# Kernel tuning notes

Hardware: AMD Instinct MI355X
Metric: run time of the kernel (lower is better)

## Reference

```python
import jax, jax.numpy as jnp
import numpy as np

E = 1024
H = 16
N, S, T = 4, 2048, 2048


def setup_inputs() -> dict:
    key = jax.random.key(0)
    ks = jax.random.split(key, 11)
    scale = 1.0 / np.sqrt(E)
    inp = {
        "query": jax.random.normal(ks[0], (N, S, E), jnp.float32),
        "key": jax.random.normal(ks[1], (N, T, E), jnp.float32),
        "value": jax.random.normal(ks[2], (N, T, E), jnp.float32),
        "Wq": jax.random.normal(ks[3], (E, E), jnp.float32) * scale,
        "bq": jax.random.normal(ks[4], (E,), jnp.float32) * 0.01,
        "Wk": jax.random.normal(ks[5], (E, E), jnp.float32) * scale,
        "bk": jax.random.normal(ks[6], (E,), jnp.float32) * 0.01,
        "Wv": jax.random.normal(ks[7], (E, E), jnp.float32) * scale,
        "bv": jax.random.normal(ks[8], (E,), jnp.float32) * 0.01,
        "Wp": jax.random.normal(ks[9], (E, E), jnp.float32) * scale,
        "bp": jax.random.normal(ks[10], (E,), jnp.float32) * 0.01,
    }
    return inp


def reference(query, key, value, Wq, bq, Wk, bk, Wv, bv, Wp, bp):
    n, s, e = query.shape
    t = value.shape[1]
    hd = e // H
    # Linear projections (torch Linear: x @ W^T + b), split into heads -> [N,H,S,hd]
    Q = (query @ Wq.T + bq).reshape(n, s, H, hd).transpose(0, 2, 1, 3)
    K = (key @ Wk.T + bk).reshape(n, t, H, hd).transpose(0, 2, 1, 3)
    V = (value @ Wv.T + bv).reshape(n, t, H, hd).transpose(0, 2, 1, 3)
    scale = 1.0 / jnp.sqrt(jnp.asarray(hd, Q.dtype))
    attn = jnp.einsum("nhsd,nhtd->nhst", Q, K) * scale  # [N,H,S,T]
    A = jax.nn.softmax(attn, axis=-1)
    Y = jnp.einsum("nhst,nhtd->nhsd", A, V)  # [N,H,S,hd]
    Y = Y.transpose(0, 2, 1, 3).reshape(n, s, e)
    return Y @ Wp.T + bp
```

## Files before the change

kernel.cpp:

```cpp
#include <hip/hip_runtime.h>
#include <hip/hip_bf16.h>
#include <stdint.h>


#define E_DIM 1024
#define H_NUM 16
#define HD 64
#define NB 4
#define SEQ 2048
#define NTOK (NB * SEQ)

typedef __bf16 bf16x8 __attribute__((ext_vector_type(8)));
typedef float f32x4 __attribute__((ext_vector_type(4)));
typedef float f32x16 __attribute__((ext_vector_type(16)));
typedef unsigned short u16;

#define MFMA16(a, b, c) __builtin_amdgcn_mfma_f32_16x16x32_bf16(a, b, c, 0, 0, 0)
#define MFMA32(a, b, c) __builtin_amdgcn_mfma_f32_32x32x16_bf16(a, b, c, 0, 0, 0)

#define VMCNT(n) asm volatile("s_waitcnt vmcnt(" #n ")" ::: "memory")
#define BAR() __builtin_amdgcn_s_barrier()
#define PRIO1() __builtin_amdgcn_s_setprio(1)
#define PRIO0() __builtin_amdgcn_s_setprio(0)

__device__ __forceinline__ u16 f2bf(float f) {
  unsigned int u = __builtin_bit_cast(unsigned int, f);
  unsigned int r = (u + 0x7FFFu + ((u >> 16) & 1u)) >> 16;
  return (u16)r;
}

__device__ __forceinline__ float fexp2(float x) {
  return __builtin_amdgcn_exp2f(x);
}

__device__ __forceinline__ void gload_lds16(const void* g, void* l) {
  __builtin_amdgcn_global_load_lds((const __attribute__((address_space(1))) void*)g,
                                   (__attribute__((address_space(3))) void*)l,
                                   16, 0, 0);
}

__device__ __forceinline__ unsigned cvtpk(float lo, float hi2) {
  unsigned w;
  asm("v_cvt_pk_bf16_f32 %0, %1, %2" : "=v"(w) : "v"(lo), "v"(hi2));
  return w;
}
__device__ __forceinline__ void plswap(unsigned& a, unsigned& b) {
  asm("v_permlane32_swap_b32 %0, %1" : "+v"(a), "+v"(b));
}

template <int B0>
__device__ __forceinline__ bf16x8 packpa(const f32x16& pe) {
  unsigned wa = cvtpk(pe[B0 + 0], pe[B0 + 1]);
  unsigned wb = cvtpk(pe[B0 + 4], pe[B0 + 5]);
  unsigned wc2 = cvtpk(pe[B0 + 2], pe[B0 + 3]);
  unsigned wd = cvtpk(pe[B0 + 6], pe[B0 + 7]);
  plswap(wa, wb);
  plswap(wc2, wd);
  union { unsigned u[4]; bf16x8 v; } pa;
  pa.u[0] = wa; pa.u[1] = wc2; pa.u[2] = wb; pa.u[3] = wd;
  return pa.v;
}

__global__ __launch_bounds__(256) void cvt7(const float* __restrict__ s0,
                                            const float* __restrict__ s1,
                                            const float* __restrict__ s2,
                                            const float* __restrict__ s3,
                                            const float* __restrict__ s4,
                                            const float* __restrict__ s5,
                                            const float* __restrict__ s6,
                                            u16* d0, u16* d1, u16* d2, u16* d3,
                                            u16* d4, u16* d5, u16* d6,
                                            int nbig, int nsmall) {
  const int t = blockIdx.y;
  const float* in;
  u16* out;
  int n4;
  switch (t) {
    case 0: in = s0; out = d0; n4 = nbig; break;
    case 1: in = s1; out = d1; n4 = nbig; break;
    case 2: in = s2; out = d2; n4 = nbig; break;
    case 3: in = s3; out = d3; n4 = nsmall; break;
    case 4: in = s4; out = d4; n4 = nsmall; break;
    case 5: in = s5; out = d5; n4 = nsmall; break;
    default: in = s6; out = d6; n4 = nsmall; break;
  }
  int idx = blockIdx.x * 256 + threadIdx.x;
  int stride = gridDim.x * 256;
  for (int i = idx; i < n4; i += stride) {
    float4 v = ((const float4*)in)[i];
    ushort4 o;
    o.x = f2bf(v.x); o.y = f2bf(v.y); o.z = f2bf(v.z); o.w = f2bf(v.w);
    ((ushort4*)out)[i] = o;
  }
}

__device__ __forceinline__ void rdA(bf16x8 (&af)[4][2], const char* pA, int off,
                                    int cs0, int cs1) {
#pragma unroll
  for (int mi = 0; mi < 4; mi++) {
    af[mi][0] = *(const bf16x8*)(pA + off + mi * 2048 + cs0);
    af[mi][1] = *(const bf16x8*)(pA + off + mi * 2048 + cs1);
  }
}
__device__ __forceinline__ void rdB(bf16x8 (&bfr)[2][2], const char* pB, int off,
                                    int cs0, int cs1) {
#pragma unroll
  for (int nj = 0; nj < 2; nj++) {
    bfr[nj][0] = *(const bf16x8*)(pB + off + nj * 2048 + cs0);
    bfr[nj][1] = *(const bf16x8*)(pB + off + nj * 2048 + cs1);
  }
}
template <int MI0, int NJ0>
__device__ __forceinline__ void mm16(f32x4 (&acc)[8][4], bf16x8 (&af)[4][2],
                                     bf16x8 (&bfr)[2][2]) {
#pragma unroll
  for (int kk = 0; kk < 2; kk++)
#pragma unroll
    for (int mi = 0; mi < 4; mi++)
#pragma unroll
      for (int nj = 0; nj < 2; nj++)
        acc[MI0 + mi][NJ0 + nj] = MFMA16(af[mi][kk], bfr[nj][kk], acc[MI0 + mi][NJ0 + nj]);
}

#define G8_SETUP(Amat, Wmat)                                                          \
  extern __shared__ char LDS[];                                                       \
  const int tid = threadIdx.x;                                                        \
  const int w = tid >> 6, l = tid & 63;                                               \
  const int lr = l & 15, lg = l >> 4;                                                 \
  const int wr = w >> 2, wc2 = w & 3;                                                 \
  const int m0 = blockIdx.x * 256;                                                    \
  const int n0g = blockIdx.y * 256;                                                   \
  const int swz = (lr & 7) << 4;                                                      \
  const int cs0 = (lg << 4) ^ swz;                                                    \
  const int cs1 = ((lg << 4) + 64) ^ swz;                                             \
  const char* pA = LDS + (wr * 16384 + lr * 128);                                     \
  const char* pB = LDS + (65536 + (wc2 >> 1) * 16384 + ((wc2 & 1) * 64 + lr) * 128);  \
  const int sr0 = tid >> 3;                                                           \
  const int sc = (((tid & 7) * 16) ^ ((sr0 & 7) << 4)) >> 1;                          \
  const u16* aS[2];                                                                   \
  const u16* bS[2];                                                                   \
  _Pragma("unroll") for (int ld = 0; ld < 2; ld++) {                                  \
    aS[ld] = (Amat) + (size_t)(m0 + ld * 64 + sr0) * E_DIM + sc;                      \
    bS[ld] = (Wmat) + (size_t)(n0g + ld * 64 + sr0) * E_DIM + sc;                     \
  }                                                                                   \
  f32x4 acc[8][4] = {};                                                               \
  bf16x8 af[4][2], bfr[2][2];

#define STG_A(h, kt)                                                                   \
  do {                                                                                 \
    const int _b = (kt) & 1;                                                           \
    gload_lds16(aS[0] + (h) * 131072 + (size_t)(kt) * 64,                              \
                LDS + _b * 32768 + (h) * 16384 + w * 1024);                            \
    gload_lds16(aS[1] + (h) * 131072 + (size_t)(kt) * 64,                              \
                LDS + _b * 32768 + (h) * 16384 + w * 1024 + 8192);                     \
  } while (0)
#define STG_B(h, kt)                                                                   \
  do {                                                                                 \
    const int _b = (kt) & 1;                                                           \
    gload_lds16(bS[0] + (h) * 131072 + (size_t)(kt) * 64,                              \
                LDS + 65536 + _b * 32768 + (h) * 16384 + w * 1024);                    \
    gload_lds16(bS[1] + (h) * 131072 + (size_t)(kt) * 64,                              \
                LDS + 65536 + _b * 32768 + (h) * 16384 + w * 1024 + 8192);             \
  } while (0)

#define FRAME(T, LAST)                                                                 \
  do {                                                                                 \
    rdA(af, pA, 0, cs0, cs1); rdB(bfr, pB, 0, cs0, cs1);                               \
    STG_B(0, (T) + 1);                                                                 \
    BAR(); PRIO1(); mm16<0, 0>(acc, af, bfr); PRIO0(); BAR();                          \
    rdB(bfr, pB, 4096, cs0, cs1);                                                      \
    STG_B(1, (T) + 1);                                                                 \
    BAR(); PRIO1(); mm16<0, 2>(acc, af, bfr); PRIO0(); BAR();                          \
    rdA(af, pA, 8192, cs0, cs1);                                                       \
    STG_A(1, (T) + 1);                                                                 \
    BAR(); PRIO1(); mm16<4, 2>(acc, af, bfr); PRIO0(); BAR();                          \
    rdB(bfr, pB, 0, cs0, cs1);                                                         \
    if (!(LAST)) { STG_A(0, (T) + 2); VMCNT(2); } else { VMCNT(0); }                   \
    BAR(); PRIO1(); mm16<4, 0>(acc, af, bfr); PRIO0(); BAR();                          \
    rdA(af, pA, 32768, cs0, cs1); rdB(bfr, pB, 32768, cs0, cs1);                       \
    if (!(LAST)) STG_B(0, (T) + 2);                                                    \
    BAR(); PRIO1(); mm16<0, 0>(acc, af, bfr); PRIO0(); BAR();                          \
    rdB(bfr, pB, 32768 + 4096, cs0, cs1);                                              \
    if (!(LAST)) STG_B(1, (T) + 2);                                                    \
    BAR(); PRIO1(); mm16<0, 2>(acc, af, bfr); PRIO0(); BAR();                          \
    rdA(af, pA, 32768 + 8192, cs0, cs1);                                               \
    if (!(LAST)) STG_A(1, (T) + 2);                                                    \
    BAR(); PRIO1(); mm16<4, 2>(acc, af, bfr); PRIO0(); BAR();                          \
    rdB(bfr, pB, 32768, cs0, cs1);                                                     \
    if (!(LAST)) { STG_A(0, (T) + 3); VMCNT(2); }                                      \
    BAR(); PRIO1(); mm16<4, 0>(acc, af, bfr); PRIO0(); BAR();                          \
  } while (0)

#define G8_LOOP()                                                                      \
  STG_A(0, 0); STG_A(1, 0); STG_B(0, 0); STG_B(1, 0); STG_A(0, 1);                     \
  VMCNT(2);                                                                            \
  BAR();                                                                               \
  _Pragma("unroll 1") for (int T = 0; T < 14; T += 2) FRAME(T, false);                 \
  FRAME(14, true);

__global__ void __launch_bounds__(512, 2) gemm_qkv8(
    const u16* __restrict__ qb, const u16* __restrict__ kb, const u16* __restrict__ vb,
    const u16* __restrict__ Wcat, const float* __restrict__ bq,
    const float* __restrict__ bk, const float* __restrict__ bv,
    u16* __restrict__ Qp, u16* __restrict__ Kp, u16* __restrict__ Vt, float qscale) {
  const int z = blockIdx.y >> 2;
  const u16* A = (z == 0) ? qb : (z == 1) ? kb : vb;
  G8_SETUP(A, Wcat);
  G8_LOOP();

  const float* bias = (z == 0) ? bq : (z == 1) ? bk : bv;
  const float osc = (z == 0) ? qscale : 1.0f;
#pragma unroll
  for (int mi = 0; mi < 8; mi++) {
#pragma unroll
    for (int nj = 0; nj < 4; nj++) {
      const int colm = (n0g + wc2 * 64 + nj * 16 + lr) & 1023;
      const float bvv = bias[colm];
      const int row0 = m0 + wr * 128 + mi * 16 + lg * 4;
      if (z == 2) {
        const int nb = row0 >> 11, t = row0 & (SEQ - 1);
        const int hh = colm >> 6, d = colm & 63;
        ushort4 o;
        o.x = f2bf(acc[mi][nj][0] + bvv);
        o.y = f2bf(acc[mi][nj][1] + bvv);
        o.z = f2bf(acc[mi][nj][2] + bvv);
        o.w = f2bf(acc[mi][nj][3] + bvv);
        *(ushort4*)&Vt[(((size_t)((nb * H_NUM + hh) * HD + d)) << 11) + t] = o;
      } else {
        u16* Cb = (z == 0) ? Qp : Kp;
#pragma unroll
        for (int ri = 0; ri < 4; ri++)
          Cb[(size_t)(row0 + ri) * E_DIM + colm] = f2bf((acc[mi][nj][ri] + bvv) * osc);
      }
    }
  }
}

__global__ void __launch_bounds__(512, 2) gemm_proj8(const u16* __restrict__ Ain,
                                                     const u16* __restrict__ W,
                                                     const float* __restrict__ bias,
                                                     float* __restrict__ Cout) {
  G8_SETUP(Ain, W);
  G8_LOOP();

#pragma unroll
  for (int mi = 0; mi < 8; mi++) {
#pragma unroll
    for (int nj = 0; nj < 4; nj++) {
      const int col = n0g + wc2 * 64 + nj * 16 + lr;
      const float bvv = bias[col];
      const int row0 = m0 + wr * 128 + mi * 16 + lg * 4;
#pragma unroll
      for (int ri = 0; ri < 4; ri++)
        Cout[(size_t)(row0 + ri) * E_DIM + col] = acc[mi][nj][ri] + bvv;
    }
  }
}
#undef FRAME
#undef STG_A
#undef STG_B
#undef G8_SETUP
#undef G8_LOOP

__global__ __launch_bounds__(256, 2) void attn_kernel(const u16* __restrict__ Qp,
                                                      const u16* __restrict__ Kp,
                                                      const u16* __restrict__ Vt,
                                                      u16* __restrict__ Yb) {
  __shared__ u16 Ks[2][64 * 64];
  __shared__ u16 Vs[2][64 * 64];
  const int h = blockIdx.x, qt = blockIdx.y, n = blockIdx.z;
  const int tid = threadIdx.x;
  const int w = tid >> 6, l = tid & 63;
  const int c = l & 31, hi = l >> 5;
  const int q0 = qt * 256 + w * 64;

  bf16x8 qfA[4], qfB[4];
  {
    const u16* qrowA = Qp + (size_t)(n * SEQ + q0 + c) * E_DIM + h * HD + hi * 8;
    const u16* qrowB = qrowA + 32 * E_DIM;
#pragma unroll
    for (int ks = 0; ks < 4; ks++) {
      qfA[ks] = *(const bf16x8*)(qrowA + ks * 16);
      qfB[ks] = *(const bf16x8*)(qrowB + ks * 16);
    }
  }

  f32x16 yA0 = {}, yA1 = {}, yB0 = {}, yB1 = {};
  float lrA = 0.f, lrB = 0.f;

  int lo[4];
#pragma unroll
  for (int ks = 0; ks < 4; ks++)
    lo[ks] = c * 128 + ((ks * 32 + hi * 16) ^ ((c & 7) << 4));

  const int sr = l >> 3;
  const int sc = ((l & 7) ^ sr) * 8;
  const u16* kgb[2];
  const u16* vgb[2];
#pragma unroll
  for (int g = 0; g < 2; g++) {
    const int row_ = (w << 4) + (g << 3) + sr;
    kgb[g] = Kp + (size_t)(n * SEQ + row_) * E_DIM + h * HD + sc;
    vgb[g] = Vt + ((size_t)((n * H_NUM + h) * HD + row_)) * SEQ + sc;
  }

#define STAGE(B, t0)                                                    \
  do {                                                                  \
    gload_lds16(kgb[0] + (size_t)(t0) * E_DIM, &Ks[B][(w << 10)]);      \
    gload_lds16(kgb[1] + (size_t)(t0) * E_DIM, &Ks[B][(w << 10) + 512]);\
    gload_lds16(vgb[0] + (t0), &Vs[B][(w << 10)]);                      \
    gload_lds16(vgb[1] + (t0), &Vs[B][(w << 10) + 512]);                \
  } while (0)

#define TILE_BODY(B)                                                           \
  do {                                                                         \
    const char* kb = (const char*)Ks[B];                                       \
    const char* vb = (const char*)Vs[B];                                       \
    f32x16 sA0 = {}, sA1 = {}, sB0 = {}, sB1 = {};                             \
    PRIO1();                                                                   \
    _Pragma("unroll") for (int ks = 0; ks < 4; ks++) {                         \
      bf16x8 ka0 = *(const bf16x8*)(kb + lo[ks]);                              \
      bf16x8 ka1 = *(const bf16x8*)(kb + lo[ks] + 4096);                       \
      sA0 = MFMA32(ka0, qfA[ks], sA0);                                         \
      sA1 = MFMA32(ka1, qfA[ks], sA1);                                         \
      sB0 = MFMA32(ka0, qfB[ks], sB0);                                         \
      sB1 = MFMA32(ka1, qfB[ks], sB1);                                         \
    }                                                                          \
    PRIO0();                                                                   \
    float pa0 = 0.f, pa1 = 0.f, pb0 = 0.f, pb1 = 0.f;                          \
    _Pragma("unroll") for (int r = 0; r < 8; r++) {                            \
      sA0[r] = fexp2(sA0[r]);         pa0 += sA0[r];                           \
      sA0[r + 8] = fexp2(sA0[r + 8]); pa1 += sA0[r + 8];                       \
      sA1[r] = fexp2(sA1[r]);         pa0 += sA1[r];                           \
      sA1[r + 8] = fexp2(sA1[r + 8]); pa1 += sA1[r + 8];                       \
      sB0[r] = fexp2(sB0[r]);         pb0 += sB0[r];                           \
      sB0[r + 8] = fexp2(sB0[r + 8]); pb1 += sB0[r + 8];                       \
      sB1[r] = fexp2(sB1[r]);         pb0 += sB1[r];                           \
      sB1[r + 8] = fexp2(sB1[r + 8]); pb1 += sB1[r + 8];                       \
    }                                                                          \
    lrA += pa0 + pa1;                                                          \
    lrB += pb0 + pb1;                                                          \
    PRIO1();                                                                   \
    _Pragma("unroll") for (int ks = 0; ks < 4; ks++) {                         \
      const f32x16& peA = (ks < 2) ? sA0 : sA1;                                \
      const f32x16& peB = (ks < 2) ? sB0 : sB1;                                \
      bf16x8 paA, paB;                                                         \
      if (ks & 1) { paA = packpa<8>(peA); paB = packpa<8>(peB); }              \
      else        { paA = packpa<0>(peA); paB = packpa<0>(peB); }              \
      bf16x8 va0 = *(const bf16x8*)(vb + lo[ks]);                              \
      bf16x8 va1 = *(const bf16x8*)(vb + lo[ks] + 4096);                       \
      yA0 = MFMA32(va0, paA, yA0);                                             \
      yA1 = MFMA32(va1, paA, yA1);                                             \
      yB0 = MFMA32(va0, paB, yB0);                                             \
      yB1 = MFMA32(va1, paB, yB1);                                             \
    }                                                                          \
    PRIO0();                                                                   \
  } while (0)

  STAGE(0, 0);
  __syncthreads();

#pragma unroll 1
  for (int it = 0; it < SEQ / 64; it += 2) {
    STAGE(1, (it + 1) * 64);
    TILE_BODY(0);
    __syncthreads();
    if (it + 2 < SEQ / 64) STAGE(0, (it + 2) * 64);
    TILE_BODY(1);
    __syncthreads();
  }

  lrA += __shfl_xor(lrA, 32, 64);
  lrB += __shfl_xor(lrB, 32, 64);
  const float invA = 1.f / lrA;
  const float invB = 1.f / lrB;
  u16* orowA = Yb + (size_t)(n * SEQ + q0 + c) * E_DIM + h * HD;
  u16* orowB = orowA + (size_t)32 * E_DIM;
#pragma unroll
  for (int df = 0; df < 2; df++) {
    const f32x16 ya = df ? yA1 : yA0;
    const f32x16 yb2 = df ? yB1 : yB0;
#pragma unroll
    for (int g = 0; g < 4; g++) {
      ushort4 oA, oB;
      oA.x = f2bf(ya[g * 4 + 0] * invA);
      oA.y = f2bf(ya[g * 4 + 1] * invA);
      oA.z = f2bf(ya[g * 4 + 2] * invA);
      oA.w = f2bf(ya[g * 4 + 3] * invA);
      oB.x = f2bf(yb2[g * 4 + 0] * invB);
      oB.y = f2bf(yb2[g * 4 + 1] * invB);
      oB.z = f2bf(yb2[g * 4 + 2] * invB);
      oB.w = f2bf(yb2[g * 4 + 3] * invB);
      *(ushort4*)(orowA + df * 32 + g * 8 + hi * 4) = oA;
      *(ushort4*)(orowB + df * 32 + g * 8 + hi * 4) = oB;
    }
  }
#undef STAGE
#undef TILE_BODY
}

extern "C" void kernel_launch(void* const* d_in, const int* in_sizes, int n_in,
                              void* d_out, int out_size, void* d_ws, size_t ws_size,
                              hipStream_t stream) {
  const float* query = (const float*)d_in[0];
  const float* key   = (const float*)d_in[1];
  const float* value = (const float*)d_in[2];
  const float* Wq = (const float*)d_in[3];
  const float* bq = (const float*)d_in[4];
  const float* Wk = (const float*)d_in[5];
  const float* bk = (const float*)d_in[6];
  const float* Wv = (const float*)d_in[7];
  const float* bv = (const float*)d_in[8];
  const float* Wp = (const float*)d_in[9];
  const float* bp = (const float*)d_in[10];

  const size_t TOK_E = (size_t)NTOK * E_DIM;
  const size_t W_E = (size_t)E_DIM * E_DIM;

  u16* ws = (u16*)d_ws;
  u16* qb  = ws;
  u16* kb  = qb + TOK_E;
  u16* vb  = kb + TOK_E;
  u16* wqb = vb + TOK_E;
  u16* wkb = wqb + W_E;
  u16* wvb = wkb + W_E;
  u16* wpb = wvb + W_E;
  u16* Qp  = wpb + W_E;
  u16* Kp  = Qp + TOK_E;
  u16* Vtb = Kp + TOK_E;
  u16* Yb  = Vtb + TOK_E;

  cvt7<<<dim3(1024, 7), 256, 0, stream>>>(query, key, value, Wq, Wk, Wv, Wp,
                                          qb, kb, vb, wqb, wkb, wvb, wpb,
                                          (int)(TOK_E / 4), (int)(W_E / 4));

  const float sc2 = 0.125f * 1.44269504088896f;

  hipFuncSetAttribute((const void*)gemm_qkv8,
                      hipFuncAttributeMaxDynamicSharedMemorySize, 131072);
  hipFuncSetAttribute((const void*)gemm_proj8,
                      hipFuncAttributeMaxDynamicSharedMemorySize, 131072);

  gemm_qkv8<<<dim3(NTOK / 256, 3072 / 256), 512, 131072, stream>>>(
      qb, kb, vb, wqb, bq, bk, bv, Qp, Kp, Vtb, sc2);

  attn_kernel<<<dim3(H_NUM, SEQ / 256, NB), 256, 0, stream>>>(Qp, Kp, Vtb, Yb);

  gemm_proj8<<<dim3(NTOK / 256, E_DIM / 256), 512, 131072, stream>>>(
      Yb, wpb, bp, (float*)d_out);
}
```

Before: 194.7 us.

## Shrink GEMM N-tile from 256 to 128 and rebuild the load pipeline

The QKV and output projection GEMMs now use 256x128 output tiles instead of 256x256. Each wave keeps 8x2 accumulators and the B-side staging loads one half-tile per k-step. The FRAME schedule and wait counts are rewritten to match, and LDS per block drops to 96KB. The intent is to launch more blocks, which helps fill the CUs on the smaller projection GEMM and may allow more residency, in exchange for lower arithmetic intensity per block and more reloading of A.

```diff
diff --git a/kernel.cpp b/kernel.cpp
--- a/kernel.cpp
+++ b/kernel.cpp
@@ -110,40 +110,40 @@
     bfr[nj][1] = *(const bf16x8*)(pB + off + nj * 2048 + cs1);
   }
 }
-template <int MI0, int NJ0>
-__device__ __forceinline__ void mm16(f32x4 (&acc)[8][4], bf16x8 (&af)[4][2],
-                                     bf16x8 (&bfr)[2][2]) {
+template <int MI0>
+__device__ __forceinline__ void mmq(f32x4 (&acc)[8][2], bf16x8 (&af)[4][2],
+                                    bf16x8 (&bfr)[2][2]) {
 #pragma unroll
   for (int kk = 0; kk < 2; kk++)
 #pragma unroll
     for (int mi = 0; mi < 4; mi++)
 #pragma unroll
       for (int nj = 0; nj < 2; nj++)
-        acc[MI0 + mi][NJ0 + nj] = MFMA16(af[mi][kk], bfr[nj][kk], acc[MI0 + mi][NJ0 + nj]);
-}
-
-#define G8_SETUP(Amat, Wmat)                                                          \
-  extern __shared__ char LDS[];                                                       \
-  const int tid = threadIdx.x;                                                        \
-  const int w = tid >> 6, l = tid & 63;                                               \
-  const int lr = l & 15, lg = l >> 4;                                                 \
-  const int wr = w >> 2, wc2 = w & 3;                                                 \
-  const int m0 = blockIdx.x * 256;                                                    \
-  const int n0g = blockIdx.y * 256;                                                   \
-  const int swz = (lr & 7) << 4;                                                      \
-  const int cs0 = (lg << 4) ^ swz;                                                    \
-  const int cs1 = ((lg << 4) + 64) ^ swz;                                             \
-  const char* pA = LDS + (wr * 16384 + lr * 128);                                     \
-  const char* pB = LDS + (65536 + (wc2 >> 1) * 16384 + ((wc2 & 1) * 64 + lr) * 128);  \
-  const int sr0 = tid >> 3;                                                           \
-  const int sc = (((tid & 7) * 16) ^ ((sr0 & 7) << 4)) >> 1;                          \
-  const u16* aS[2];                                                                   \
-  const u16* bS[2];                                                                   \
-  _Pragma("unroll") for (int ld = 0; ld < 2; ld++) {                                  \
-    aS[ld] = (Amat) + (size_t)(m0 + ld * 64 + sr0) * E_DIM + sc;                      \
-    bS[ld] = (Wmat) + (size_t)(n0g + ld * 64 + sr0) * E_DIM + sc;                     \
-  }                                                                                   \
-  f32x4 acc[8][4] = {};                                                               \
+        acc[MI0 + mi][nj] = MFMA16(af[mi][kk], bfr[nj][kk], acc[MI0 + mi][nj]);
+}
+
+#define G8_SETUP(Amat, Wmat)                                                      \
+  extern __shared__ char LDS[];                                                   \
+  const int tid = threadIdx.x;                                                    \
+  const int w = tid >> 6, l = tid & 63;                                           \
+  const int lr = l & 15, lg = l >> 4;                                             \
+  const int wr = w >> 2, wc2 = w & 3;                                             \
+  const int m0 = blockIdx.x * 256;                                                \
+  const int n0g = blockIdx.y * 128;                                               \
+  const int swz = (lr & 7) << 4;                                                  \
+  const int cs0 = (lg << 4) ^ swz;                                                \
+  const int cs1 = ((lg << 4) + 64) ^ swz;                                         \
+  const char* pA = LDS + (wr * 16384 + lr * 128);                                 \
+  const char* pB = LDS + (65536 + (wc2 * 32 + lr) * 128);                         \
+  const int sr0 = tid >> 3;                                                       \
+  const int sc = (((tid & 7) * 16) ^ ((sr0 & 7) << 4)) >> 1;                      \
+  const u16* aS[2];                                                               \
+  const u16* bS[2];                                                               \
+  _Pragma("unroll") for (int ld = 0; ld < 2; ld++) {                              \
+    aS[ld] = (Amat) + (size_t)(m0 + ld * 64 + sr0) * E_DIM + sc;                  \
+    bS[ld] = (Wmat) + (size_t)(n0g + ld * 64 + sr0) * E_DIM + sc;                 \
+  }                                                                               \
+  f32x4 acc[8][2] = {};                                                           \
   bf16x8 af[4][2], bfr[2][2];
 
 #define STG_A(h, kt)                                                                   \
@@ -154,46 +154,40 @@
     gload_lds16(aS[1] + (h) * 131072 + (size_t)(kt) * 64,                              \
                 LDS + _b * 32768 + (h) * 16384 + w * 1024 + 8192);                     \
   } while (0)
-#define STG_B(h, kt)                                                                   \
+#define STG_B(kt)                                                                      \
   do {                                                                                 \
     const int _b = (kt) & 1;                                                           \
-    gload_lds16(bS[0] + (h) * 131072 + (size_t)(kt) * 64,                              \
-                LDS + 65536 + _b * 32768 + (h) * 16384 + w * 1024);                    \
-    gload_lds16(bS[1] + (h) * 131072 + (size_t)(kt) * 64,                              \
-                LDS + 65536 + _b * 32768 + (h) * 16384 + w * 1024 + 8192);             \
+    gload_lds16(bS[0] + (size_t)(kt) * 64,                                             \
+                LDS + 65536 + _b * 16384 + w * 1024);                                  \
+    gload_lds16(bS[1] + (size_t)(kt) * 64,                                             \
+                LDS + 65536 + _b * 16384 + w * 1024 + 8192);                           \
   } while (0)
 
 #define FRAME(T, LAST)                                                                 \
   do {                                                                                 \
-    rdA(af, pA, 0, cs0, cs1); rdB(bfr, pB, 0, cs0, cs1);                               \
-    STG_B(0, (T) + 1);                                                                 \
-    BAR(); PRIO1(); mm16<0, 0>(acc, af, bfr); PRIO0(); BAR();                          \
-    rdB(bfr, pB, 4096, cs0, cs1);                                                      \
-    STG_B(1, (T) + 1);                                                                 \
-    BAR(); PRIO1(); mm16<0, 2>(acc, af, bfr); PRIO0(); BAR();                          \
+                                                      \
+    rdA(af, pA, 0, cs0, cs1);                                                          \
+    rdB(bfr, pB, 0, cs0, cs1);                                                         \
+    STG_A(1, (T) + 1);                                                                 \
+    BAR(); PRIO1(); mmq<0>(acc, af, bfr); PRIO0(); BAR();                              \
+                                                             \
     rdA(af, pA, 8192, cs0, cs1);                                                       \
-    STG_A(1, (T) + 1);                                                                 \
-    BAR(); PRIO1(); mm16<4, 2>(acc, af, bfr); PRIO0(); BAR();                          \
-    rdB(bfr, pB, 0, cs0, cs1);                                                         \
-    if (!(LAST)) { STG_A(0, (T) + 2); VMCNT(2); } else { VMCNT(0); }                   \
-    BAR(); PRIO1(); mm16<4, 0>(acc, af, bfr); PRIO0(); BAR();                          \
-    rdA(af, pA, 32768, cs0, cs1); rdB(bfr, pB, 32768, cs0, cs1);                       \
-    if (!(LAST)) STG_B(0, (T) + 2);                                                    \
-    BAR(); PRIO1(); mm16<0, 0>(acc, af, bfr); PRIO0(); BAR();                          \
-    rdB(bfr, pB, 32768 + 4096, cs0, cs1);                                              \
-    if (!(LAST)) STG_B(1, (T) + 2);                                                    \
-    BAR(); PRIO1(); mm16<0, 2>(acc, af, bfr); PRIO0(); BAR();                          \
+    if (!(LAST)) { STG_B((T) + 2); VMCNT(2); } else { VMCNT(0); }                      \
+    BAR(); PRIO1(); mmq<4>(acc, af, bfr); PRIO0(); BAR();                              \
+                                                    \
+    rdA(af, pA, 32768, cs0, cs1);                                                      \
+    rdB(bfr, pB, 16384, cs0, cs1);                                                     \
+    if (!(LAST)) { STG_A(0, (T) + 2); STG_A(1, (T) + 2); }                             \
+    BAR(); PRIO1(); mmq<0>(acc, af, bfr); PRIO0(); BAR();                              \
+                                                           \
     rdA(af, pA, 32768 + 8192, cs0, cs1);                                               \
-    if (!(LAST)) STG_A(1, (T) + 2);                                                    \
-    BAR(); PRIO1(); mm16<4, 2>(acc, af, bfr); PRIO0(); BAR();                          \
-    rdB(bfr, pB, 32768, cs0, cs1);                                                     \
-    if (!(LAST)) { STG_A(0, (T) + 3); VMCNT(2); }                                      \
-    BAR(); PRIO1(); mm16<4, 0>(acc, af, bfr); PRIO0(); BAR();                          \
+    if (!(LAST)) { STG_B((T) + 3); STG_A(0, (T) + 3); VMCNT(4); }                      \
+    BAR(); PRIO1(); mmq<4>(acc, af, bfr); PRIO0(); BAR();                              \
   } while (0)
 
 #define G8_LOOP()                                                                      \
-  STG_A(0, 0); STG_A(1, 0); STG_B(0, 0); STG_B(1, 0); STG_A(0, 1);                     \
-  VMCNT(2);                                                                            \
+  STG_B(0); STG_A(0, 0); STG_A(1, 0); STG_B(1); STG_A(0, 1);                           \
+  VMCNT(4);                                                                            \
   BAR();                                                                               \
   _Pragma("unroll 1") for (int T = 0; T < 14; T += 2) FRAME(T, false);                 \
   FRAME(14, true);
@@ -203,7 +197,7 @@
     const u16* __restrict__ Wcat, const float* __restrict__ bq,
     const float* __restrict__ bk, const float* __restrict__ bv,
     u16* __restrict__ Qp, u16* __restrict__ Kp, u16* __restrict__ Vt, float qscale) {
-  const int z = blockIdx.y >> 2;
+  const int z = blockIdx.y >> 3;
   const u16* A = (z == 0) ? qb : (z == 1) ? kb : vb;
   G8_SETUP(A, Wcat);
   G8_LOOP();
@@ -213,8 +207,8 @@
 #pragma unroll
   for (int mi = 0; mi < 8; mi++) {
 #pragma unroll
-    for (int nj = 0; nj < 4; nj++) {
-      const int colm = (n0g + wc2 * 64 + nj * 16 + lr) & 1023;
+    for (int nj = 0; nj < 2; nj++) {
+      const int colm = (n0g + wc2 * 32 + nj * 16 + lr) & 1023;
       const float bvv = bias[colm];
       const int row0 = m0 + wr * 128 + mi * 16 + lg * 4;
       if (z == 2) {
@@ -246,8 +240,8 @@
 #pragma unroll
   for (int mi = 0; mi < 8; mi++) {
 #pragma unroll
-    for (int nj = 0; nj < 4; nj++) {
-      const int col = n0g + wc2 * 64 + nj * 16 + lr;
+    for (int nj = 0; nj < 2; nj++) {
+      const int col = n0g + wc2 * 32 + nj * 16 + lr;
       const float bvv = bias[col];
       const int row0 = m0 + wr * 128 + mi * 16 + lg * 4;
 #pragma unroll
@@ -437,15 +431,15 @@
   const float sc2 = 0.125f * 1.44269504088896f;
 
   hipFuncSetAttribute((const void*)gemm_qkv8,
-                      hipFuncAttributeMaxDynamicSharedMemorySize, 131072);
+                      hipFuncAttributeMaxDynamicSharedMemorySize, 98304);
   hipFuncSetAttribute((const void*)gemm_proj8,
-                      hipFuncAttributeMaxDynamicSharedMemorySize, 131072);
-
-  gemm_qkv8<<<dim3(NTOK / 256, 3072 / 256), 512, 131072, stream>>>(
+                      hipFuncAttributeMaxDynamicSharedMemorySize, 98304);
+
+  gemm_qkv8<<<dim3(NTOK / 256, 3072 / 128), 512, 98304, stream>>>(
       qb, kb, vb, wqb, bq, bk, bv, Qp, Kp, Vtb, sc2);
 
   attn_kernel<<<dim3(H_NUM, SEQ / 256, NB), 256, 0, stream>>>(Qp, Kp, Vtb, Yb);
 
-  gemm_proj8<<<dim3(NTOK / 256, E_DIM / 256), 512, 131072, stream>>>(
+  gemm_proj8<<<dim3(NTOK / 256, E_DIM / 128), 512, 98304, stream>>>(
       Yb, wpb, bp, (float*)d_out);
 }
```

After: 177.0 us. 9.1% less time.
